# Kernel optimization log

Hardware: AMD Instinct MI355X
Metric: run time of the kernel (lower is better)

The kernel has to match this reference:

```python
import jax, jax.numpy as jnp
import numpy as np

M, N, D = 100000, 64, 128  # points, channels, voxel grid side


def setup_inputs() -> dict:
    key = jax.random.key(0)
    k1, k2, k3, k4, k5 = jax.random.split(key, 5)
    rng = np.random.default_rng(0)
    # unique occupied voxels in a D^3 grid (Minkowski coords are unique)
    lin = rng.choice(D ** 3, size=M, replace=False)
    coords = np.stack(np.unravel_index(lin, (D, D, D)), axis=1).astype(np.int32)
    w_scale = 0.02  # ~1/sqrt(fan_in=27*N)
    return {
        "feats": jax.random.normal(k1, (M, N), dtype=jnp.float32),
        "W1": jax.random.normal(k2, (27, N, N), dtype=jnp.float32) * w_scale,
        "b1": jax.random.normal(k3, (N,), dtype=jnp.float32) * 0.01,
        "W2": jax.random.normal(k4, (27, N, N), dtype=jnp.float32) * w_scale,
        "b2": jax.random.normal(k5, (N,), dtype=jnp.float32) * 0.01,
        "coords": jnp.asarray(coords),
        "grid_size": D,
    }


def reference(feats, W1, b1, W2, b2, coords, grid_size):
    Dg = grid_size
    m = feats.shape[0]
    # dense hash: linear voxel id -> point index (-1 if empty)
    lin = (coords[:, 0].astype(jnp.int32) * Dg + coords[:, 1]) * Dg + coords[:, 2]
    lookup = jnp.full((Dg * Dg * Dg,), -1, dtype=jnp.int32).at[lin].set(
        jnp.arange(m, dtype=jnp.int32))
    offsets = jnp.array([[i, j, k] for i in (-1, 0, 1) for j in (-1, 0, 1)
                         for k in (-1, 0, 1)], dtype=jnp.int32)  # [27,3]

    def sparse_conv(x, W, b):
        # out[u] = b + sum_k W_k^T gather(x, u+off_k); scan over 27 offsets keeps
        # only one [M,N] gathered buffer live (memory-bound gather-GEMM-scatter)
        def step(acc, wk_off):
            W_k, off = wk_off
            nc = coords + off  # [M,3]
            inb = jnp.all((nc >= 0) & (nc < Dg), axis=1)
            nlin = (nc[:, 0] * Dg + nc[:, 1]) * Dg + nc[:, 2]
            nidx = lookup[jnp.where(inb, nlin, 0)]
            valid = inb & (nidx >= 0)
            g = jnp.where(valid[:, None], x[jnp.maximum(nidx, 0)], 0.0)  # [M,N]
            return acc + g @ W_k, None
        init = jnp.zeros_like(x) + b
        out, _ = jax.lax.scan(step, init, (W, offsets))
        return out

    h = jax.nn.relu(sparse_conv(feats, W1, b1))
    return jax.nn.relu(sparse_conv(h, W2, b2))
```

## Files before the change

kernel.cpp:

```cpp
#include <hip/hip_runtime.h>
#include <hip/hip_bf16.h>
#include <cstdint>
#include <cstddef>

typedef _Float16 half8 __attribute__((ext_vector_type(8)));
typedef float floatx16 __attribute__((ext_vector_type(16)));

#define DGRID 128
#define D3 (DGRID * DGRID * DGRID)
#define WSZ (2 * 27 * 4096)

struct __attribute__((aligned(4))) I3 { int a, b, c; };

__global__ void prep(const int* __restrict__ coords, const float* __restrict__ feats,
                     const float* __restrict__ W1, const float* __restrict__ W2,
                     int* __restrict__ lookup, _Float16* __restrict__ Whf,
                     _Float16* __restrict__ h0, _Float16* __restrict__ h, int M) {
    int tid = blockIdx.x * 256 + threadIdx.x;
    if (tid < WSZ) {
        int idx = tid;
        int j = idx & 7;
        int l = (idx >> 3) & 63;
        int f = (idx >> 9) & 7;
        int kL = idx >> 12;
        int k = kL % 27, L = kL / 27;
        int kk = f & 3, ct = f >> 2;
        int c = kk * 16 + (l >> 5) * 8 + j;
        int n = ct * 32 + (l & 31);
        const float* W = L ? W2 : W1;
        Whf[idx] = (_Float16)W[k * 4096 + c * 64 + n];
        return;
    }
    tid -= WSZ;
    if (tid < M) {
        int x = coords[3 * tid], y = coords[3 * tid + 1], z = coords[3 * tid + 2];
        lookup[(x * DGRID + y) * DGRID + z] = tid;
        return;
    }
    tid -= M;
    if (tid < 64) {
        h0[(size_t)M * 64 + tid] = (_Float16)0.f;
        h[(size_t)M * 64 + tid] = (_Float16)0.f;
        return;
    }
    tid -= 64;
    if (tid < M * 8) {
        const float4* src = (const float4*)feats + (size_t)tid * 2;
        float4 f0 = src[0], f1 = src[1];
        half8 v;
        v[0] = (_Float16)f0.x; v[1] = (_Float16)f0.y;
        v[2] = (_Float16)f0.z; v[3] = (_Float16)f0.w;
        v[4] = (_Float16)f1.x; v[5] = (_Float16)f1.y;
        v[6] = (_Float16)f1.z; v[7] = (_Float16)f1.w;
        ((half8*)h0)[tid] = v;
    }
}

template <bool FIRST, bool OUT_F16>
__global__ __launch_bounds__(64, 2) void spconv(const _Float16* __restrict__ x,
                                                const _Float16* __restrict__ Whf,
                                                const float* __restrict__ bias,
                                                const int* __restrict__ coords,
                                                const int* __restrict__ lookup,
                                                int* __restrict__ nbr,
                                                void* __restrict__ outp, int M) {
    __shared__ int nvs[27 * 64];
    __shared__ _Float16 abuf[2][4096];
    const int lane = threadIdx.x;
    const int lrow = lane & 31;
    const int lhalf = lane >> 5;
    const int r8 = lane >> 3;
    const int c8 = lane & 7;
    const int mw = blockIdx.x * 64;

    {
        const int row = mw + lane;
        if constexpr (FIRST) {
            if (row < M) {
                int X = coords[3 * row], Y = coords[3 * row + 1], Z = coords[3 * row + 2];
                int zlo = Z - 1;
                if (zlo < 0) zlo = 0;
                if (zlo > DGRID - 3) zlo = DGRID - 3;
                const int zi = Z - zlo;
#pragma unroll
                for (int dx = -1; dx <= 1; ++dx)
#pragma unroll
                    for (int dy = -1; dy <= 1; ++dy) {
                        int nx = X + dx, ny = Y + dy;
                        int v0 = -1, v1 = -1, v2 = -1;
                        if (((unsigned)nx < DGRID) && ((unsigned)ny < DGRID)) {
                            I3 t = *(const I3*)(lookup + ((nx * DGRID + ny) * DGRID + zlo));
                            v0 = t.a; v1 = t.b; v2 = t.c;
                        }
#pragma unroll
                        for (int dz = -1; dz <= 1; ++dz) {
                            int zc = Z + dz;
                            int i = zi + dz;
                            int val = (i == 0) ? v0 : (i == 1) ? v1 : v2;
                            int nidx = M;
                            if (((unsigned)zc < DGRID) && ((unsigned)val < (unsigned)M))
                                nidx = val;
                            int k = (dx + 1) * 9 + (dy + 1) * 3 + (dz + 1);
                            nvs[k * 64 + lane] = nidx;
                            nbr[(size_t)k * M + row] = nidx;
                        }
                    }
            } else {
#pragma unroll
                for (int k = 0; k < 27; ++k) nvs[k * 64 + lane] = M;
            }
        } else {
            const int rc = row < M ? row : M - 1;
#pragma unroll
            for (int k = 0; k < 27; ++k) nvs[k * 64 + lane] = nbr[(size_t)k * M + rc];
        }
    }
    __syncthreads();

    floatx16 acc[4];
#pragma unroll
    for (int i = 0; i < 4; ++i)
#pragma unroll
        for (int j = 0; j < 16; ++j) acc[i][j] = 0.0f;

    const half8* wb = (const half8*)Whf + lane;

    auto loadB = [&](half8* dst, int k) {
#pragma unroll
        for (int f = 0; f < 8; ++f) dst[f] = wb[(k * 8 + f) * 64];
    };

    auto stageA = [&](int buf, int k) {
#pragma unroll
        for (int s = 0; s < 8; ++s) {
            int nv = nvs[k * 64 + s * 8 + r8];
            const _Float16* src = x + (size_t)nv * 64 + (c8 ^ r8) * 8;
            __builtin_amdgcn_global_load_lds(
                (const __attribute__((address_space(1))) void*)src,
                (__attribute__((address_space(3))) void*)&abuf[buf][s * 512],
                16, 0, 0);
        }
    };

    auto readA = [&](half8* dst, int buf, int rt) {
        const _Float16* base = &abuf[buf][(rt * 32 + lrow) * 64];
        const int key = lrow & 7;
#pragma unroll
        for (int kk = 0; kk < 4; ++kk) {
            int slot = (lhalf + kk * 2) ^ key;
            dst[kk] = *(const half8*)(base + slot * 8);
        }
    };

    half8 Br[2][8];
    stageA(0, 0);
    loadB(Br[0], 0);

#pragma unroll
    for (int i = 0; i < 27; ++i) {
        if (i + 1 < 27) {
            stageA((i + 1) & 1, i + 1);
            loadB(Br[(i + 1) & 1], i + 1);
        }
        __builtin_amdgcn_sched_barrier(0);
        if (i + 1 < 27)
            asm volatile("s_waitcnt vmcnt(16)" ::: "memory");
        else
            asm volatile("s_waitcnt vmcnt(0)" ::: "memory");
        __builtin_amdgcn_sched_barrier(0);
        half8 a0[4], a1[4];
        readA(a0, i & 1, 0);
        readA(a1, i & 1, 1);
        half8* B = Br[i & 1];
#pragma unroll
        for (int kk = 0; kk < 4; ++kk)
#pragma unroll
            for (int ct = 0; ct < 2; ++ct) {
                acc[0 * 2 + ct] = __builtin_amdgcn_mfma_f32_32x32x16_f16(
                    a0[kk], B[ct * 4 + kk], acc[0 * 2 + ct], 0, 0, 0);
                acc[1 * 2 + ct] = __builtin_amdgcn_mfma_f32_32x32x16_f16(
                    a1[kk], B[ct * 4 + kk], acc[1 * 2 + ct], 0, 0, 0);
            }
    }

    const float bv0 = bias[lrow], bv1 = bias[32 + lrow];
#pragma unroll
    for (int rt = 0; rt < 2; ++rt)
#pragma unroll
        for (int ct = 0; ct < 2; ++ct) {
            const float bb = ct ? bv1 : bv0;
#pragma unroll
            for (int reg = 0; reg < 16; ++reg) {
                int row = (reg & 3) + 8 * (reg >> 2) + 4 * lhalf;
                int g = mw + rt * 32 + row;
                if (g < M) {
                    float v = acc[rt * 2 + ct][reg] + bb;
                    v = v > 0.f ? v : 0.f;
                    size_t off = (size_t)g * 64 + ct * 32 + lrow;
                    if constexpr (OUT_F16)
                        ((_Float16*)outp)[off] = (_Float16)v;
                    else
                        ((float*)outp)[off] = v;
                }
            }
        }
}

extern "C" void kernel_launch(void* const* d_in, const int* in_sizes, int n_in,
                              void* d_out, int out_size, void* d_ws, size_t ws_size,
                              hipStream_t stream) {
    const float* feats = (const float*)d_in[0];
    const float* W1 = (const float*)d_in[1];
    const float* b1 = (const float*)d_in[2];
    const float* W2 = (const float*)d_in[3];
    const float* b2 = (const float*)d_in[4];
    const int* coords = (const int*)d_in[5];
    const int M = in_sizes[0] / 64;

    int* lookup = (int*)d_ws;
    int* nbr = lookup + (size_t)D3;
    _Float16* h = (_Float16*)(nbr + (size_t)27 * M);
    _Float16* h0 = h + (size_t)(M + 1) * 64;
    _Float16* Whf = h0 + (size_t)(M + 1) * 64;
    size_t need = (size_t)D3 * 4 + (size_t)27 * M * 4 +
                  2 * (size_t)(M + 1) * 64 * 2 + (size_t)WSZ * 2;
    if (ws_size < need) return;

    long long pt = (long long)WSZ + M + 64 + (long long)M * 8;
    prep<<<(int)((pt + 255) / 256), 256, 0, stream>>>(coords, feats, W1, W2, lookup, Whf,
                                                      h0, h, M);

    int cb = (M + 63) / 64;
    spconv<true, true><<<cb, 64, 0, stream>>>(h0, Whf, b1, coords, lookup, nbr,
                                              (void*)h, M);
    spconv<false, false><<<cb, 64, 0, stream>>>(h, Whf + (size_t)27 * 4096, b2, coords,
                                                lookup, nbr, d_out, M);
}
```

Measured before the change: 200.3 us.

## Use two-wave 128-row blocks with barrier-based sync in sparse conv

Each sparse-conv block now covers 128 output rows with two waves, each wave owning its own 64-row slice of the neighbor table and LDS staging buffer. The hand-placed s_waitcnt vmcnt(16) pipelining is replaced by __syncthreads after the A-tile reads in every offset iteration. The waves share no data, so the barriers add cross-wave coupling. The barrier will probably drain all outstanding loads, including the prefetch for the next offset, which risks losing the overlap between global gathers and MFMA work.

```diff
diff --git a/kernel.cpp b/kernel.cpp
--- a/kernel.cpp
+++ b/kernel.cpp
@@ -57,24 +57,27 @@
 }
 
 template <bool FIRST, bool OUT_F16>
-__global__ __launch_bounds__(64, 2) void spconv(const _Float16* __restrict__ x,
-                                                const _Float16* __restrict__ Whf,
-                                                const float* __restrict__ bias,
-                                                const int* __restrict__ coords,
-                                                const int* __restrict__ lookup,
-                                                int* __restrict__ nbr,
-                                                void* __restrict__ outp, int M) {
-    __shared__ int nvs[27 * 64];
-    __shared__ _Float16 abuf[2][4096];
-    const int lane = threadIdx.x;
+__global__ __launch_bounds__(128, 2) void spconv(const _Float16* __restrict__ x,
+                                                 const _Float16* __restrict__ Whf,
+                                                 const float* __restrict__ bias,
+                                                 const int* __restrict__ coords,
+                                                 const int* __restrict__ lookup,
+                                                 int* __restrict__ nbr,
+                                                 void* __restrict__ outp, int M) {
+    __shared__ int nvs[27 * 128];
+    __shared__ _Float16 abuf[2][128 * 64];
+    const int tid = threadIdx.x;
+    const int lane = tid & 63;
+    const int wid = tid >> 6;
     const int lrow = lane & 31;
     const int lhalf = lane >> 5;
     const int r8 = lane >> 3;
     const int c8 = lane & 7;
-    const int mw = blockIdx.x * 64;
+    const int mw = blockIdx.x * 128;
+    const int wrow = wid * 64;
 
     {
-        const int row = mw + lane;
+        const int row = mw + tid;
         if constexpr (FIRST) {
             if (row < M) {
                 int X = coords[3 * row], Y = coords[3 * row + 1], Z = coords[3 * row + 2];
@@ -101,18 +104,18 @@
                             if (((unsigned)zc < DGRID) && ((unsigned)val < (unsigned)M))
                                 nidx = val;
                             int k = (dx + 1) * 9 + (dy + 1) * 3 + (dz + 1);
-                            nvs[k * 64 + lane] = nidx;
+                            nvs[k * 128 + tid] = nidx;
                             nbr[(size_t)k * M + row] = nidx;
                         }
                     }
             } else {
 #pragma unroll
-                for (int k = 0; k < 27; ++k) nvs[k * 64 + lane] = M;
+                for (int k = 0; k < 27; ++k) nvs[k * 128 + tid] = M;
             }
         } else {
             const int rc = row < M ? row : M - 1;
 #pragma unroll
-            for (int k = 0; k < 27; ++k) nvs[k * 64 + lane] = nbr[(size_t)k * M + rc];
+            for (int k = 0; k < 27; ++k) nvs[k * 128 + tid] = nbr[(size_t)k * M + rc];
         }
     }
     __syncthreads();
@@ -133,17 +136,18 @@
     auto stageA = [&](int buf, int k) {
 #pragma unroll
         for (int s = 0; s < 8; ++s) {
-            int nv = nvs[k * 64 + s * 8 + r8];
+            int rr = wrow + s * 8 + r8;
+            int nv = nvs[k * 128 + rr];
             const _Float16* src = x + (size_t)nv * 64 + (c8 ^ r8) * 8;
             __builtin_amdgcn_global_load_lds(
                 (const __attribute__((address_space(1))) void*)src,
-                (__attribute__((address_space(3))) void*)&abuf[buf][s * 512],
+                (__attribute__((address_space(3))) void*)&abuf[buf][(wrow + s * 8) * 64],
                 16, 0, 0);
         }
     };
 
     auto readA = [&](half8* dst, int buf, int rt) {
-        const _Float16* base = &abuf[buf][(rt * 32 + lrow) * 64];
+        const _Float16* base = &abuf[buf][(wrow + rt * 32 + lrow) * 64];
         const int key = lrow & 7;
 #pragma unroll
         for (int kk = 0; kk < 4; ++kk) {
@@ -155,6 +159,7 @@
     half8 Br[2][8];
     stageA(0, 0);
     loadB(Br[0], 0);
+    __syncthreads();
 
 #pragma unroll
     for (int i = 0; i < 27; ++i) {
@@ -162,15 +167,11 @@
             stageA((i + 1) & 1, i + 1);
             loadB(Br[(i + 1) & 1], i + 1);
         }
-        __builtin_amdgcn_sched_barrier(0);
-        if (i + 1 < 27)
-            asm volatile("s_waitcnt vmcnt(16)" ::: "memory");
-        else
-            asm volatile("s_waitcnt vmcnt(0)" ::: "memory");
-        __builtin_amdgcn_sched_barrier(0);
         half8 a0[4], a1[4];
         readA(a0, i & 1, 0);
         readA(a1, i & 1, 1);
+        __builtin_amdgcn_sched_barrier(0);
+        __syncthreads();
         half8* B = Br[i & 1];
 #pragma unroll
         for (int kk = 0; kk < 4; ++kk)
@@ -192,7 +193,7 @@
 #pragma unroll
             for (int reg = 0; reg < 16; ++reg) {
                 int row = (reg & 3) + 8 * (reg >> 2) + 4 * lhalf;
-                int g = mw + rt * 32 + row;
+                int g = mw + wrow + rt * 32 + row;
                 if (g < M) {
                     float v = acc[rt * 2 + ct][reg] + bb;
                     v = v > 0.f ? v : 0.f;
@@ -230,9 +231,9 @@
     prep<<<(int)((pt + 255) / 256), 256, 0, stream>>>(coords, feats, W1, W2, lookup, Whf,
                                                       h0, h, M);
 
-    int cb = (M + 63) / 64;
-    spconv<true, true><<<cb, 64, 0, stream>>>(h0, Whf, b1, coords, lookup, nbr,
-                                              (void*)h, M);
-    spconv<false, false><<<cb, 64, 0, stream>>>(h, Whf + (size_t)27 * 4096, b2, coords,
-                                                lookup, nbr, d_out, M);
+    int cb = (M + 127) / 128;
+    spconv<true, true><<<cb, 128, 0, stream>>>(h0, Whf, b1, coords, lookup, nbr,
+                                               (void*)h, M);
+    spconv<false, false><<<cb, 128, 0, stream>>>(h, Whf + (size_t)27 * 4096, b2, coords,
+                                                 lookup, nbr, d_out, M);
 }
```

New measurement: 215.3 us. 1.07x slower.

## Stage gathered rows through registers with triple LDS buffering and deeper prefetch

Applied to the files above, without the earlier changes.

Neighbor-row gathers no longer use direct global-to-LDS loads. Rows are now loaded into registers two offsets ahead, then written into one of three swizzled LDS buffers one offset ahead, and the hand-written vmcnt waits are removed so the compiler places the waits. The goal is to hide more of the irregular gather latency behind the MFMA work. The cost is extra VGPRs for the staged rows, which may limit occupancy under the two-waves launch bound, plus explicit LDS write instructions and more LDS space.

```diff
diff --git a/kernel.cpp b/kernel.cpp
--- a/kernel.cpp
+++ b/kernel.cpp
@@ -65,12 +65,12 @@
                                                 int* __restrict__ nbr,
                                                 void* __restrict__ outp, int M) {
     __shared__ int nvs[27 * 64];
-    __shared__ _Float16 abuf[2][4096];
+    __shared__ _Float16 abuf[3][64 * 64];
     const int lane = threadIdx.x;
     const int lrow = lane & 31;
     const int lhalf = lane >> 5;
-    const int r8 = lane >> 3;
-    const int c8 = lane & 7;
+    const int srow = lane >> 3;
+    const int schk = lane & 7;
     const int mw = blockIdx.x * 64;
 
     {
@@ -130,47 +130,44 @@
         for (int f = 0; f < 8; ++f) dst[f] = wb[(k * 8 + f) * 64];
     };
 
-    auto stageA = [&](int buf, int k) {
+    auto gload = [&](half8* g, int k) {
 #pragma unroll
         for (int s = 0; s < 8; ++s) {
-            int nv = nvs[k * 64 + s * 8 + r8];
-            const _Float16* src = x + (size_t)nv * 64 + (c8 ^ r8) * 8;
-            __builtin_amdgcn_global_load_lds(
-                (const __attribute__((address_space(1))) void*)src,
-                (__attribute__((address_space(3))) void*)&abuf[buf][s * 512],
-                16, 0, 0);
-        }
-    };
-
+            int nv = nvs[k * 64 + s * 8 + srow];
+            g[s] = *(const half8*)(x + (size_t)nv * 64 + schk * 8);
+        }
+    };
+    auto swrite = [&](int buf, half8* g) {
+        _Float16* bp = abuf[buf];
+#pragma unroll
+        for (int s = 0; s < 8; ++s)
+            *(half8*)(bp + (size_t)(s * 8 + srow) * 64 + (schk ^ srow) * 8) = g[s];
+    };
     auto readA = [&](half8* dst, int buf, int rt) {
-        const _Float16* base = &abuf[buf][(rt * 32 + lrow) * 64];
+        const _Float16* base = abuf[buf] + (size_t)(rt * 32 + lrow) * 64;
         const int key = lrow & 7;
 #pragma unroll
-        for (int kk = 0; kk < 4; ++kk) {
-            int slot = (lhalf + kk * 2) ^ key;
-            dst[kk] = *(const half8*)(base + slot * 8);
-        }
-    };
-
-    half8 Br[2][8];
-    stageA(0, 0);
+        for (int kk = 0; kk < 4; ++kk)
+            dst[kk] = *(const half8*)(base + ((lhalf + kk * 2) ^ key) * 8);
+    };
+
+    half8 G[2][8], Br[2][8];
+    gload(G[0], 0);
+    gload(G[1], 1);
     loadB(Br[0], 0);
+    swrite(0, G[0]);
 
 #pragma unroll
     for (int i = 0; i < 27; ++i) {
+        if (i + 2 < 27) gload(G[i & 1], i + 2);
         if (i + 1 < 27) {
-            stageA((i + 1) & 1, i + 1);
+            swrite((i + 1) % 3, G[(i + 1) & 1]);
             loadB(Br[(i + 1) & 1], i + 1);
         }
+        half8 a0[4], a1[4];
+        readA(a0, i % 3, 0);
+        readA(a1, i % 3, 1);
         __builtin_amdgcn_sched_barrier(0);
-        if (i + 1 < 27)
-            asm volatile("s_waitcnt vmcnt(16)" ::: "memory");
-        else
-            asm volatile("s_waitcnt vmcnt(0)" ::: "memory");
-        __builtin_amdgcn_sched_barrier(0);
-        half8 a0[4], a1[4];
-        readA(a0, i & 1, 0);
-        readA(a1, i & 1, 1);
         half8* B = Br[i & 1];
 #pragma unroll
         for (int kk = 0; kk < 4; ++kk)
```

Measured after the change: 205.5 us. 2.6% more time.
